# Performance work log

Measured on AMD Instinct MI355X. Metric: run time of the kernel, lower is better.

Reference implementation:

```python
import math
import jax, jax.numpy as jnp
import numpy as np
from jax import lax

BIG = 1e20
HUGE = 1e30
SMALL = 1e-10
EPSILON = 0.1
NITER = 50
B, I, J = 256, 256, 256


def setup_inputs() -> dict:
    key = jax.random.key(0)
    # normalized word-pair distances in [0, 1)
    D = jax.random.uniform(key, (B, I, J), dtype=jnp.float32)
    return {"D": D}


def _kl_div(x, y):
    div = x / (y + SMALL)
    return y * (div * jnp.log(div + SMALL) - div + 1.0)


def _wfr_forward(D, epsilon, niter):
    pi2 = jnp.float32(math.pi / 2)
    C = -2.0 * jnp.log(jnp.cos(jnp.minimum(D * 2.0, pi2)) + 1e-5)  # [B,I,J]
    b_, i_, j_ = C.shape
    dx = 1.0 / i_  # uniform weights 1/I
    dy = 1.0 / j_  # uniform weights 1/J
    p_coef = 1.0 / (1.0 + epsilon)

    def K_calc(u, v):
        # K = clamp(exp((-C + u_i + v_j)/eps))
        return jnp.clip(jnp.exp((-C + u[:, :, None] + v[:, None, :]) / epsilon), 0.0, HUGE)

    b0 = jnp.ones((b_, j_), C.dtype)
    u0 = jnp.zeros((b_, i_), C.dtype)
    v0 = jnp.zeros((b_, j_), C.dtype)
    K0 = K_calc(u0, v0)

    def body(ii, carry):
        b, u, v, K = carry
        # row update: s_i = sum_j K_ij * b_j * dy ; mu = 1
        s = jnp.sum(K * (b * dy)[:, None, :], axis=-1)  # [B,I]
        a = jnp.clip((1.0 / (jnp.exp(u) * s)) ** p_coef, 0.0, HUGE)
        # col update: s_j = sum_i K_ij * a_i * dx ; nu = 1
        s2 = jnp.sum(K * (a * dx)[:, :, None], axis=-2)  # [B,J]
        b_new = jnp.clip((1.0 / (jnp.exp(v) * s2)) ** p_coef, 0.0, HUGE)

        rescale = (jnp.max(a) > BIG) | (jnp.max(b_new) > BIG) | (ii == niter - 1)

        def do_rescale(_):
            u2 = epsilon * jnp.log(a) + u
            v2 = epsilon * jnp.log(b_new) + v
            return jnp.ones_like(b_new), u2, v2, K_calc(u2, v2)

        def no_rescale(_):
            return b_new, u, v, K

        return lax.cond(rescale, do_rescale, no_rescale, None)

    b, u, v, K = lax.fori_loop(0, niter, body, (b0, u0, v0, K0))

    # marginal constraint penalties (KL against uniform mu=nu=1)
    row_marg = jnp.sum(K * dy, axis=-1)            # [B,I]
    cons1 = jnp.sum(_kl_div(row_marg, 1.0) * dx, axis=-1)
    col_marg = jnp.sum(K * dx, axis=-2)            # [B,J]
    cons2 = jnp.sum(_kl_div(col_marg, 1.0) * dy, axis=-1)
    transport = jnp.sum(K * C, axis=(-2, -1)) * dx * dy
    p_opt = cons1 + cons2 + transport               # [B]
    return p_opt, K


def reference(D):
    p_opt, _K = _wfr_forward(D, EPSILON, NITER)
    return p_opt
```

## Files before the change

kernel.cpp:

```cpp
#include <hip/hip_runtime.h>
#include <hip/hip_fp16.h>
#include <math.h>

#define NITERS 50

typedef _Float16 h2_t __attribute__((ext_vector_type(2)));

#if defined(__has_builtin)
#if __has_builtin(__builtin_amdgcn_fdot2)
#define HAVE_FDOT2 1
#endif
#endif

__device__ __forceinline__ float fdot2f(unsigned int ka, unsigned int kb, float acc) {
#ifdef HAVE_FDOT2
    return __builtin_amdgcn_fdot2(__builtin_bit_cast(h2_t, ka),
                                  __builtin_bit_cast(h2_t, kb), acc, false);
#else
    h2_t a = __builtin_bit_cast(h2_t, ka);
    h2_t b = __builtin_bit_cast(h2_t, kb);
    return acc + (float)a.x * (float)b.x + (float)a.y * (float)b.y;
#endif
}

__global__ __launch_bounds__(512, 2) void wfr_kernel(const float* __restrict__ D,
                                                     float* __restrict__ out) {
    __shared__ __align__(16) __half Ksh[256 * 256];
    __shared__ __align__(16) float  sh_bf[256];
    __shared__ __align__(16) float  sh_af[256];
    __shared__ __align__(16) float  sh_s2[256];
    __shared__ __align__(16) __half sh_bh[256];
    __shared__ __align__(16) float  part[512];
    __shared__ __align__(16) float  cpart[4096];

    const int tid = threadIdx.x;
    const int bb  = blockIdx.x;
    char* Kbytes  = reinterpret_cast<char*>(Ksh);

    {
        const float4* D4 = reinterpret_cast<const float4*>(D + (size_t)bb * 65536);
        for (int k = 0; k < 32; ++k) {
            int idx4 = tid + (k << 9);
            float4 d = D4[idx4];
            int i = idx4 >> 6;
            int j = (idx4 & 63) << 2;
            float v0[4] = {d.x, d.y, d.z, d.w};
            float k0[4];
            #pragma unroll
            for (int q = 0; q < 4; ++q) {
                float c = cosf(fminf(v0[q] * 2.0f, 1.57079632679489662f)) + 1e-5f;
                k0[q] = expf(20.0f * logf(c));
            }
            h2_t h01 = { (_Float16)k0[0], (_Float16)k0[1] };
            h2_t h23 = { (_Float16)k0[2], (_Float16)k0[3] };
            uint2 wv;
            wv.x = __builtin_bit_cast(unsigned int, h01);
            wv.y = __builtin_bit_cast(unsigned int, h23);
            int off = (i << 9) + (((j << 1) ^ ((i & 31) << 4)));
            *reinterpret_cast<uint2*>(Kbytes + off) = wv;
        }
    }
    if (tid < 256) {
        sh_bf[tid] = 1.0f;
        sh_bh[tid] = __float2half(1.0f);
    }
    __syncthreads();

    const int r   = tid & 255;
    const int hh  = tid >> 8;
    const int rsw = r & 31;
    const char* Krow = Kbytes + (r << 9);
    const int g   = tid & 31;
    const int hc  = tid >> 5;

    uint4 krow4[16];
    #pragma unroll
    for (int c = 0; c < 16; ++c) {
        int chunk = (hh << 4) + c;
        krow4[c] = *reinterpret_cast<const uint4*>(Krow + ((chunk ^ rsw) << 4));
    }
    uint4 kcol4[16];
    #pragma unroll
    for (int m = 0; m < 16; ++m) {
        int i = (hc << 4) + m;
        kcol4[m] = *reinterpret_cast<const uint4*>(
            Kbytes + (i << 9) + ((g ^ (i & 31)) << 4));
    }

    for (int it = 0; it < NITERS; ++it) {
        float s0 = 0.0f, s1 = 0.0f, s2a = 0.0f, s3 = 0.0f;
        #pragma unroll
        for (int c = 0; c < 16; ++c) {
            uint4 bv = *reinterpret_cast<const uint4*>(
                reinterpret_cast<const char*>(sh_bh) + (((hh << 4) + c) << 4));
            s0  = fdot2f(krow4[c].x, bv.x, s0);
            s1  = fdot2f(krow4[c].y, bv.y, s1);
            s2a = fdot2f(krow4[c].z, bv.z, s2a);
            s3  = fdot2f(krow4[c].w, bv.w, s3);
        }
        part[tid] = (s0 + s1) + (s2a + s3);
        __syncthreads();
        if (tid < 256) {
            float sf = (part[tid] + part[tid + 256]) * (1.0f / 256.0f);
            float a  = __powf(1.0f / sf, 1.0f / 1.1f);
            a = fminf(a, 1e30f);
            sh_af[tid] = a;
        }
        __syncthreads();

        float f0=0,f1=0,f2=0,f3=0,f4=0,f5=0,f6=0,f7=0;
        #pragma unroll
        for (int m = 0; m < 16; ++m) {
            float ai = sh_af[(hc << 4) + m];
            h2_t p0 = __builtin_bit_cast(h2_t, kcol4[m].x);
            h2_t p1 = __builtin_bit_cast(h2_t, kcol4[m].y);
            h2_t p2 = __builtin_bit_cast(h2_t, kcol4[m].z);
            h2_t p3 = __builtin_bit_cast(h2_t, kcol4[m].w);
            f0 = fmaf((float)p0.x, ai, f0);
            f1 = fmaf((float)p0.y, ai, f1);
            f2 = fmaf((float)p1.x, ai, f2);
            f3 = fmaf((float)p1.y, ai, f3);
            f4 = fmaf((float)p2.x, ai, f4);
            f5 = fmaf((float)p2.y, ai, f5);
            f6 = fmaf((float)p3.x, ai, f6);
            f7 = fmaf((float)p3.y, ai, f7);
        }
        {
            float* cp = cpart + (hc << 8) + (g << 3);
            *reinterpret_cast<float4*>(cp)     = make_float4(f0, f1, f2, f3);
            *reinterpret_cast<float4*>(cp + 4) = make_float4(f4, f5, f6, f7);
        }
        __syncthreads();
        if (tid < 256) {
            float s2 = 0.0f;
            #pragma unroll
            for (int q = 0; q < 16; ++q) s2 += cpart[(q << 8) + tid];
            s2 *= (1.0f / 256.0f);
            float bn = __powf(1.0f / s2, 1.0f / 1.1f);
            bn = fminf(bn, 1e30f);
            sh_bf[tid] = bn;
            sh_bh[tid] = __float2half(bn);
            sh_s2[tid] = s2;
        }
        __syncthreads();
    }

    {
        float s = 0.0f, tp = 0.0f;
        #pragma unroll
        for (int c = 0; c < 16; ++c) {
            int chunk = (hh << 4) + c;
            float4 blo = *reinterpret_cast<const float4*>(sh_bf + (chunk << 3));
            float4 bhi = *reinterpret_cast<const float4*>(sh_bf + (chunk << 3) + 4);
            h2_t p0 = __builtin_bit_cast(h2_t, krow4[c].x);
            h2_t p1 = __builtin_bit_cast(h2_t, krow4[c].y);
            h2_t p2 = __builtin_bit_cast(h2_t, krow4[c].z);
            h2_t p3 = __builtin_bit_cast(h2_t, krow4[c].w);
            float kf[8] = {(float)p0.x,(float)p0.y,(float)p1.x,(float)p1.y,
                           (float)p2.x,(float)p2.y,(float)p3.x,(float)p3.y};
            float bf[8] = {blo.x,blo.y,blo.z,blo.w,bhi.x,bhi.y,bhi.z,bhi.w};
            #pragma unroll
            for (int q = 0; q < 8; ++q) {
                float prod = kf[q] * bf[q];
                s += prod;
                float cl = (kf[q] > 0.0f) ? (-0.1f * __logf(kf[q])) : 0.0f;
                tp = fmaf(prod, cl, tp);
            }
        }
        part[tid]  = s;
        cpart[tid] = tp;
    }
    __syncthreads();
    float val = 0.0f;
    if (tid < 256) {
        float sfin     = (part[tid] + part[tid + 256]) * (1.0f / 256.0f);
        float af       = sh_af[tid];
        float row_marg = af * sfin;
        float col_marg = sh_bf[tid] * sh_s2[tid];
        float tprow    = af * (cpart[tid] + cpart[tid + 256]);
        float d1  = row_marg / (1.0f + 1e-10f);
        float kl1 = d1 * __logf(d1 + 1e-10f) - d1 + 1.0f;
        float d2  = col_marg / (1.0f + 1e-10f);
        float kl2 = d2 * __logf(d2 + 1e-10f) - d2 + 1.0f;
        val = (kl1 + kl2) * (1.0f / 256.0f) + tprow * (1.0f / 65536.0f);
    }
    __syncthreads();
    part[tid] = val;
    __syncthreads();
    for (int off = 256; off > 0; off >>= 1) {
        if (tid < off) part[tid] += part[tid + off];
        __syncthreads();
    }
    if (tid == 0) out[bb] = part[0];
}

extern "C" void kernel_launch(void* const* d_in, const int* in_sizes, int n_in,
                              void* d_out, int out_size, void* d_ws, size_t ws_size,
                              hipStream_t stream) {
    (void)in_sizes; (void)n_in; (void)d_ws; (void)ws_size; (void)out_size;
    const float* D = reinterpret_cast<const float*>(d_in[0]);
    float* out     = reinterpret_cast<float*>(d_out);
    wfr_kernel<<<dim3(256), dim3(512), 0, stream>>>(D, out);
}
```

Before: 204.5 us.

## Split block into row and column thread groups with full-row/column K in registers

Threads 0-255 each hold a full K row and threads 256-511 each hold a full K column in registers, so each half computes its sums with fdot2 over the whole row or column. This removes the cross-thread partial-sum shared buffers and one barrier per iteration, and turns the column update from scalar fp32 FMAs into packed fp16 dot products using a half-precision copy of a. The cost is that each half idles while the other phase runs, and the column loads at setup are strided 2-byte LDS reads. The final reduction now uses wavefront shuffles.

```diff
diff --git a/kernel.cpp b/kernel.cpp
--- a/kernel.cpp
+++ b/kernel.cpp
@@ -27,11 +27,9 @@
                                                      float* __restrict__ out) {
     __shared__ __align__(16) __half Ksh[256 * 256];
     __shared__ __align__(16) float  sh_bf[256];
-    __shared__ __align__(16) float  sh_af[256];
-    __shared__ __align__(16) float  sh_s2[256];
     __shared__ __align__(16) __half sh_bh[256];
-    __shared__ __align__(16) float  part[512];
-    __shared__ __align__(16) float  cpart[4096];
+    __shared__ __align__(16) __half sh_ah[256];
+    __shared__ __align__(16) float  part[8];
 
     const int tid = threadIdx.x;
     const int bb  = blockIdx.x;
@@ -66,96 +64,87 @@
     }
     __syncthreads();
 
-    const int r   = tid & 255;
-    const int hh  = tid >> 8;
-    const int rsw = r & 31;
-    const char* Krow = Kbytes + (r << 9);
-    const int g   = tid & 31;
-    const int hc  = tid >> 5;
+    const bool is_row = (tid < 256);
+    const int  r  = tid & 255;
 
-    uint4 krow4[16];
-    #pragma unroll
-    for (int c = 0; c < 16; ++c) {
-        int chunk = (hh << 4) + c;
-        krow4[c] = *reinterpret_cast<const uint4*>(Krow + ((chunk ^ rsw) << 4));
-    }
-    uint4 kcol4[16];
-    #pragma unroll
-    for (int m = 0; m < 16; ++m) {
-        int i = (hc << 4) + m;
-        kcol4[m] = *reinterpret_cast<const uint4*>(
-            Kbytes + (i << 9) + ((g ^ (i & 31)) << 4));
+    uint4 kreg[32];
+    if (is_row) {
+        const char* Krow = Kbytes + (r << 9);
+        const int rsw = r & 31;
+        #pragma unroll
+        for (int c = 0; c < 32; ++c)
+            kreg[c] = *reinterpret_cast<const uint4*>(Krow + ((c ^ rsw) << 4));
+    } else {
+        #pragma unroll
+        for (int c = 0; c < 32; ++c) {
+            unsigned int w[4];
+            #pragma unroll
+            for (int h = 0; h < 4; ++h) {
+                int i0 = (c << 3) + (h << 1);
+                int i1 = i0 + 1;
+                unsigned int lo = *reinterpret_cast<const unsigned short*>(
+                    Kbytes + (i0 << 9) + ((r << 1) ^ ((i0 & 31) << 4)));
+                unsigned int hi = *reinterpret_cast<const unsigned short*>(
+                    Kbytes + (i1 << 9) + ((r << 1) ^ ((i1 & 31) << 4)));
+                w[h] = lo | (hi << 16);
+            }
+            kreg[c].x = w[0]; kreg[c].y = w[1]; kreg[c].z = w[2]; kreg[c].w = w[3];
+        }
     }
 
+    float a_local = 0.0f, b_local = 0.0f, s2m_local = 0.0f;
+
     for (int it = 0; it < NITERS; ++it) {
-        float s0 = 0.0f, s1 = 0.0f, s2a = 0.0f, s3 = 0.0f;
-        #pragma unroll
-        for (int c = 0; c < 16; ++c) {
-            uint4 bv = *reinterpret_cast<const uint4*>(
-                reinterpret_cast<const char*>(sh_bh) + (((hh << 4) + c) << 4));
-            s0  = fdot2f(krow4[c].x, bv.x, s0);
-            s1  = fdot2f(krow4[c].y, bv.y, s1);
-            s2a = fdot2f(krow4[c].z, bv.z, s2a);
-            s3  = fdot2f(krow4[c].w, bv.w, s3);
-        }
-        part[tid] = (s0 + s1) + (s2a + s3);
-        __syncthreads();
-        if (tid < 256) {
-            float sf = (part[tid] + part[tid + 256]) * (1.0f / 256.0f);
-            float a  = __powf(1.0f / sf, 1.0f / 1.1f);
+        if (is_row) {
+            float s0 = 0.0f, s1 = 0.0f, sa = 0.0f, sb = 0.0f;
+            #pragma unroll
+            for (int c = 0; c < 32; ++c) {
+                uint4 bv = *reinterpret_cast<const uint4*>(
+                    reinterpret_cast<const char*>(sh_bh) + (c << 4));
+                s0 = fdot2f(kreg[c].x, bv.x, s0);
+                s1 = fdot2f(kreg[c].y, bv.y, s1);
+                sa = fdot2f(kreg[c].z, bv.z, sa);
+                sb = fdot2f(kreg[c].w, bv.w, sb);
+            }
+            float sf = ((s0 + s1) + (sa + sb)) * (1.0f / 256.0f);
+            float a  = __powf(sf, -(1.0f / 1.1f));
             a = fminf(a, 1e30f);
-            sh_af[tid] = a;
+            a_local = a;
+            sh_ah[r] = __float2half(a);
         }
         __syncthreads();
-
-        float f0=0,f1=0,f2=0,f3=0,f4=0,f5=0,f6=0,f7=0;
-        #pragma unroll
-        for (int m = 0; m < 16; ++m) {
-            float ai = sh_af[(hc << 4) + m];
-            h2_t p0 = __builtin_bit_cast(h2_t, kcol4[m].x);
-            h2_t p1 = __builtin_bit_cast(h2_t, kcol4[m].y);
-            h2_t p2 = __builtin_bit_cast(h2_t, kcol4[m].z);
-            h2_t p3 = __builtin_bit_cast(h2_t, kcol4[m].w);
-            f0 = fmaf((float)p0.x, ai, f0);
-            f1 = fmaf((float)p0.y, ai, f1);
-            f2 = fmaf((float)p1.x, ai, f2);
-            f3 = fmaf((float)p1.y, ai, f3);
-            f4 = fmaf((float)p2.x, ai, f4);
-            f5 = fmaf((float)p2.y, ai, f5);
-            f6 = fmaf((float)p3.x, ai, f6);
-            f7 = fmaf((float)p3.y, ai, f7);
-        }
-        {
-            float* cp = cpart + (hc << 8) + (g << 3);
-            *reinterpret_cast<float4*>(cp)     = make_float4(f0, f1, f2, f3);
-            *reinterpret_cast<float4*>(cp + 4) = make_float4(f4, f5, f6, f7);
-        }
-        __syncthreads();
-        if (tid < 256) {
-            float s2 = 0.0f;
+        if (!is_row) {
+            float s0 = 0.0f, s1 = 0.0f, sa = 0.0f, sb = 0.0f;
             #pragma unroll
-            for (int q = 0; q < 16; ++q) s2 += cpart[(q << 8) + tid];
-            s2 *= (1.0f / 256.0f);
-            float bn = __powf(1.0f / s2, 1.0f / 1.1f);
+            for (int c = 0; c < 32; ++c) {
+                uint4 av = *reinterpret_cast<const uint4*>(
+                    reinterpret_cast<const char*>(sh_ah) + (c << 4));
+                s0 = fdot2f(kreg[c].x, av.x, s0);
+                s1 = fdot2f(kreg[c].y, av.y, s1);
+                sa = fdot2f(kreg[c].z, av.z, sa);
+                sb = fdot2f(kreg[c].w, av.w, sb);
+            }
+            s2m_local = ((s0 + s1) + (sa + sb)) * (1.0f / 256.0f);
+            float bn = __powf(s2m_local, -(1.0f / 1.1f));
             bn = fminf(bn, 1e30f);
-            sh_bf[tid] = bn;
-            sh_bh[tid] = __float2half(bn);
-            sh_s2[tid] = s2;
+            b_local = bn;
+            sh_bf[r] = bn;
+            sh_bh[r] = __float2half(bn);
         }
         __syncthreads();
     }
 
-    {
+    float val;
+    if (is_row) {
         float s = 0.0f, tp = 0.0f;
         #pragma unroll
-        for (int c = 0; c < 16; ++c) {
-            int chunk = (hh << 4) + c;
-            float4 blo = *reinterpret_cast<const float4*>(sh_bf + (chunk << 3));
-            float4 bhi = *reinterpret_cast<const float4*>(sh_bf + (chunk << 3) + 4);
-            h2_t p0 = __builtin_bit_cast(h2_t, krow4[c].x);
-            h2_t p1 = __builtin_bit_cast(h2_t, krow4[c].y);
-            h2_t p2 = __builtin_bit_cast(h2_t, krow4[c].z);
-            h2_t p3 = __builtin_bit_cast(h2_t, krow4[c].w);
+        for (int c = 0; c < 32; ++c) {
+            float4 blo = *reinterpret_cast<const float4*>(sh_bf + (c << 3));
+            float4 bhi = *reinterpret_cast<const float4*>(sh_bf + (c << 3) + 4);
+            h2_t p0 = __builtin_bit_cast(h2_t, kreg[c].x);
+            h2_t p1 = __builtin_bit_cast(h2_t, kreg[c].y);
+            h2_t p2 = __builtin_bit_cast(h2_t, kreg[c].z);
+            h2_t p3 = __builtin_bit_cast(h2_t, kreg[c].w);
             float kf[8] = {(float)p0.x,(float)p0.y,(float)p1.x,(float)p1.y,
                            (float)p2.x,(float)p2.y,(float)p3.x,(float)p3.y};
             float bf[8] = {blo.x,blo.y,blo.z,blo.w,bhi.x,bhi.y,bhi.z,bhi.w};
@@ -167,31 +156,28 @@
                 tp = fmaf(prod, cl, tp);
             }
         }
-        part[tid]  = s;
-        cpart[tid] = tp;
-    }
-    __syncthreads();
-    float val = 0.0f;
-    if (tid < 256) {
-        float sfin     = (part[tid] + part[tid + 256]) * (1.0f / 256.0f);
-        float af       = sh_af[tid];
-        float row_marg = af * sfin;
-        float col_marg = sh_bf[tid] * sh_s2[tid];
-        float tprow    = af * (cpart[tid] + cpart[tid + 256]);
+        float row_marg = a_local * s * (1.0f / 256.0f);
         float d1  = row_marg / (1.0f + 1e-10f);
         float kl1 = d1 * __logf(d1 + 1e-10f) - d1 + 1.0f;
+        val = kl1 * (1.0f / 256.0f) + (a_local * tp) * (1.0f / 65536.0f);
+    } else {
+        float col_marg = b_local * s2m_local;
         float d2  = col_marg / (1.0f + 1e-10f);
         float kl2 = d2 * __logf(d2 + 1e-10f) - d2 + 1.0f;
-        val = (kl1 + kl2) * (1.0f / 256.0f) + tprow * (1.0f / 65536.0f);
+        val = kl2 * (1.0f / 256.0f);
     }
+
+    #pragma unroll
+    for (int off = 32; off > 0; off >>= 1)
+        val += __shfl_down(val, off, 64);
+    if ((tid & 63) == 0) part[tid >> 6] = val;
     __syncthreads();
-    part[tid] = val;
-    __syncthreads();
-    for (int off = 256; off > 0; off >>= 1) {
-        if (tid < off) part[tid] += part[tid + off];
-        __syncthreads();
+    if (tid == 0) {
+        float t = 0.0f;
+        #pragma unroll
+        for (int w = 0; w < 8; ++w) t += part[w];
+        out[bb] = t;
     }
-    if (tid == 0) out[bb] = part[0];
 }
 
 extern "C" void kernel_launch(void* const* d_in, const int* in_sizes, int n_in,
```

After: 216.7 us. 1.06x slower.
